# Optimization experiments

Hardware: AMD Instinct MI355X
Metric: run time of the kernel (lower is better)

Reference implementation:

```python
import jax, jax.numpy as jnp
import numpy as np

B, L, H2 = 64, 512, 1024  # batch, question length, 2*hidden_dim


def setup_inputs() -> dict:
    key = jax.random.key(0)
    ks = jax.random.split(key, 9)
    sc = 1.0 / np.sqrt(H2)
    return {
        "s_t_hat": jax.random.normal(ks[0], (B, H2), dtype=jnp.float32),
        "pai_q": jax.random.normal(ks[1], (B, L, H2), dtype=jnp.float32),
        "que_padding_mask": (jax.random.uniform(ks[2], (B, L)) > 0.1).astype(jnp.float32),
        "que_coverage": jax.random.uniform(ks[3], (B, L), dtype=jnp.float32),
        "W_q": jax.random.normal(ks[4], (H2, H2), dtype=jnp.float32) * sc,
        "W_qs_w": jax.random.normal(ks[5], (H2, H2), dtype=jnp.float32) * sc,
        "W_qs_b": jax.random.normal(ks[6], (H2,), dtype=jnp.float32) * sc,
        "W_c": jax.random.normal(ks[7], (1, H2), dtype=jnp.float32) * sc,
        "v_q": jax.random.normal(ks[8], (H2, 1), dtype=jnp.float32) * sc,
    }


def reference(s_t_hat, pai_q, que_padding_mask, que_coverage, W_q, W_qs_w, W_qs_b, W_c, v_q):
    # encoder feature: (b, l, 2h)
    enc_feat = jnp.einsum("blh,hk->blk", pai_q, W_q)
    # decoder feature: (b, 2h) -> broadcast over l
    dec_feat = s_t_hat @ W_qs_w + W_qs_b
    att = enc_feat + dec_feat[:, None, :]
    # coverage feature: (b, l, 1) @ (1, 2h)
    att = att + que_coverage[:, :, None] * W_c[0][None, None, :]
    e = jnp.tanh(att)                                  # (b, l, 2h)
    scores = jnp.einsum("blh,ho->bl", e, v_q)          # (b, l)
    alpha = jax.nn.softmax(scores, axis=1) * que_padding_mask
    alpha = alpha / jnp.sum(alpha, axis=1, keepdims=True)
    c_q_t = jnp.einsum("bl,blh->bh", alpha, pai_q)      # (b, 2h)
    new_cov = que_coverage + alpha
    return (c_q_t, alpha, new_cov)
```

## Files before the change

### kernel.cpp

```cpp
#include <hip/hip_runtime.h>
#include <hip/hip_bf16.h>

#define B_   64
#define L_   512
#define H2_  1024
#define M_   (B_ * L_)
#define KSPLIT 16
#define KCH  (H2_ / KSPLIT)

typedef short bf16x8 __attribute__((ext_vector_type(8)));
typedef float f32x4  __attribute__((ext_vector_type(4)));
typedef ushort ushort8_t __attribute__((ext_vector_type(8)));

__device__ __forceinline__ ushort f2bf(float f) {
    uint x = __float_as_uint(f);
    uint r = (x + 0x7FFFu + ((x >> 16) & 1u)) >> 16;
    return (ushort)r;
}

__device__ __forceinline__ float fast_tanh(float x) {
    float ax = fabsf(x);
    float e  = __expf(-2.0f * ax);
    float t  = 1.0f - 2.0f * e / (1.0f + e);
    return copysignf(t, x);
}

__device__ __forceinline__ void gload_lds16(const ushort* g, ushort* l) {
    __builtin_amdgcn_global_load_lds(
        (const __attribute__((address_space(1))) void*)g,
        (__attribute__((address_space(3))) void*)l, 16, 0, 0);
}

__global__ __launch_bounds__(256) void convertA_kernel(
    const float* __restrict__ in, ushort* __restrict__ out)
{
    size_t i = ((size_t)blockIdx.x * 256 + threadIdx.x) * 8;
    float4 a = *(const float4*)&in[i];
    float4 b = *(const float4*)&in[i + 4];
    ushort8_t h;
    h[0] = f2bf(a.x); h[1] = f2bf(a.y); h[2] = f2bf(a.z); h[3] = f2bf(a.w);
    h[4] = f2bf(b.x); h[5] = f2bf(b.y); h[6] = f2bf(b.z); h[7] = f2bf(b.w);
    *(ushort8_t*)&out[i] = h;
}

__global__ __launch_bounds__(256) void convertB_kernel(
    const float* __restrict__ W, ushort* __restrict__ out)
{
    __shared__ float t[32][33];
    int tx = threadIdx.x & 31, ty = threadIdx.x >> 5;
    int k0 = blockIdx.x * 32, n0 = blockIdx.y * 32;
    #pragma unroll
    for (int r = 0; r < 4; ++r)
        t[ty + r * 8][tx] = W[(size_t)(k0 + ty + r * 8) * H2_ + n0 + tx];
    __syncthreads();
    #pragma unroll
    for (int r = 0; r < 4; ++r)
        out[(size_t)(n0 + ty + r * 8) * H2_ + k0 + tx] = f2bf(t[tx][ty + r * 8]);
}

__global__ __launch_bounds__(256) void dec_split_kernel(
    const float* __restrict__ s_t_hat, const float* __restrict__ Wqs,
    float* __restrict__ dec_part)
{
    const int t  = threadIdx.x;
    const int n  = blockIdx.x * 64 + (t & 63);
    const int k0 = blockIdx.y * KCH;
    const int bg = t >> 6;

    float acc[16];
    #pragma unroll
    for (int i = 0; i < 16; ++i) acc[i] = 0.f;

    for (int k8 = 0; k8 < KCH; k8 += 8) {
        float w[8];
        #pragma unroll
        for (int kk = 0; kk < 8; ++kk)
            w[kk] = Wqs[(size_t)(k0 + k8 + kk) * H2_ + n];
        #pragma unroll
        for (int i = 0; i < 16; ++i) {
            const float* srow = &s_t_hat[(bg * 16 + i) * H2_ + k0 + k8];
            #pragma unroll
            for (int kk = 0; kk < 8; ++kk)
                acc[i] += srow[kk] * w[kk];
        }
    }
    #pragma unroll
    for (int i = 0; i < 16; ++i)
        dec_part[(size_t)blockIdx.y * (B_ * H2_) + (bg * 16 + i) * H2_ + n] = acc[i];
}

__global__ __launch_bounds__(256) void dec_reduce_kernel(
    const float* __restrict__ dec_part, const float* __restrict__ bqs,
    float* __restrict__ dec)
{
    int i = blockIdx.x * 256 + threadIdx.x;
    float s = bqs[i & (H2_ - 1)];
    #pragma unroll
    for (int p = 0; p < KSPLIT; ++p) s += dec_part[(size_t)p * (B_ * H2_) + i];
    dec[i] = s;
}

__global__ __launch_bounds__(256) void dec_kernel(
    const float* __restrict__ s_t_hat, const float* __restrict__ Wqs,
    const float* __restrict__ bqs, float* __restrict__ dec)
{
    int n  = blockIdx.x * 256 + threadIdx.x;
    int b0 = blockIdx.y * 4;
    float a0 = 0.f, a1 = 0.f, a2 = 0.f, a3 = 0.f;
    for (int h = 0; h < H2_; ++h) {
        float w = Wqs[h * H2_ + n];
        a0 += s_t_hat[(b0 + 0) * H2_ + h] * w;
        a1 += s_t_hat[(b0 + 1) * H2_ + h] * w;
        a2 += s_t_hat[(b0 + 2) * H2_ + h] * w;
        a3 += s_t_hat[(b0 + 3) * H2_ + h] * w;
    }
    float bias = bqs[n];
    dec[(b0 + 0) * H2_ + n] = a0 + bias;
    dec[(b0 + 1) * H2_ + n] = a1 + bias;
    dec[(b0 + 2) * H2_ + n] = a2 + bias;
    dec[(b0 + 3) * H2_ + n] = a3 + bias;
}

#define BM 128
#define BN 128
#define BK 64

__global__ __launch_bounds__(256) void score_kernel3(
    const ushort* __restrict__ Abf,
    const ushort* __restrict__ Bbf,
    const float* __restrict__ dec,
    const float* __restrict__ cov,
    const float* __restrict__ Wc,
    const float* __restrict__ vq,
    float* __restrict__ scores_part)
{
    __shared__ ushort As[BM * BK];
    __shared__ ushort Bs[BN * BK];

    const int tid  = threadIdx.x;
    const int lane = tid & 63;
    const int wave = tid >> 6;
    const int wm = wave >> 1, wn = wave & 1;
    const int m0 = blockIdx.x * BM;
    const int n0 = blockIdx.y * BN;

    f32x4 acc[4][4] = {};

    const int srow = lane >> 3;
    const int scol = ((lane & 7) ^ srow) * 8;
    const size_t abase = (size_t)(m0 + wave * 32 + srow) * H2_ + scol;
    const size_t bbase = (size_t)(n0 + wave * 32 + srow) * H2_ + scol;
    ushort* lA = As + wave * 32 * BK;
    ushort* lB = Bs + wave * 32 * BK;

    const int fr = lane & 15;
    const int fg = lane >> 4;
    const int fx = fr & 7;

    for (int kt = 0; kt < H2_; kt += BK) {
        #pragma unroll
        for (int p = 0; p < 4; ++p) {
            gload_lds16(Abf + abase + p * 8 * H2_ + kt, lA + p * 8 * BK);
            gload_lds16(Bbf + bbase + p * 8 * H2_ + kt, lB + p * 8 * BK);
        }
        __syncthreads();

        bf16x8 af[4][2];
        #pragma unroll
        for (int i = 0; i < 4; ++i)
            #pragma unroll
            for (int ks = 0; ks < 2; ++ks)
                af[i][ks] = *(const bf16x8*)
                    &As[(wm * 64 + i * 16 + fr) * BK + (((fg + ks * 4) ^ fx) * 8)];

        #pragma unroll
        for (int j = 0; j < 4; ++j) {
            bf16x8 b0 = *(const bf16x8*)
                &Bs[(wn * 64 + j * 16 + fr) * BK + ((fg ^ fx) * 8)];
            bf16x8 b1 = *(const bf16x8*)
                &Bs[(wn * 64 + j * 16 + fr) * BK + (((fg + 4) ^ fx) * 8)];
            #pragma unroll
            for (int i = 0; i < 4; ++i) {
                acc[i][j] = __builtin_amdgcn_mfma_f32_16x16x32_bf16(af[i][0], b0, acc[i][j], 0, 0, 0);
                acc[i][j] = __builtin_amdgcn_mfma_f32_16x16x32_bf16(af[i][1], b1, acc[i][j], 0, 0, 0);
            }
        }
        __syncthreads();
    }

    const int b = m0 >> 9;
    float dec4[4], wc4[4], vq4[4];
    #pragma unroll
    for (int j = 0; j < 4; ++j) {
        int n = n0 + wn * 64 + j * 16 + fr;
        dec4[j] = dec[b * H2_ + n];
        wc4[j]  = Wc[n];
        vq4[j]  = vq[n];
    }
    #pragma unroll
    for (int i = 0; i < 4; ++i) {
        #pragma unroll
        for (int r = 0; r < 4; ++r) {
            int ml = wm * 64 + i * 16 + fg * 4 + r;
            int m  = m0 + ml;
            float cv = cov[b * L_ + (m & (L_ - 1))];
            float s = 0.f;
            #pragma unroll
            for (int j = 0; j < 4; ++j) {
                float att = acc[i][j][r] + dec4[j] + cv * wc4[j];
                s += fast_tanh(att) * vq4[j];
            }
            s += __shfl_xor(s, 1);
            s += __shfl_xor(s, 2);
            s += __shfl_xor(s, 4);
            s += __shfl_xor(s, 8);
            if (fr == 0)
                scores_part[(size_t)(blockIdx.y * 2 + wn) * M_ + m] = s;
        }
    }
}

#define LDK 40
__global__ __launch_bounds__(256) void score_kernel_fb(
    const float* __restrict__ A, const float* __restrict__ Bmat,
    const float* __restrict__ dec, const float* __restrict__ cov,
    const float* __restrict__ Wc, const float* __restrict__ vq,
    float* __restrict__ scores_part)
{
    __shared__ ushort As[BM * LDK];
    __shared__ ushort Bs[BN * LDK];
    const int tid  = threadIdx.x;
    const int lane = tid & 63;
    const int wave = tid >> 6;
    const int wm = wave >> 1, wn = wave & 1;
    const int m0 = blockIdx.x * BM;
    const int n0 = blockIdx.y * BN;
    f32x4 acc[4][4] = {};
    const int a_row = tid >> 3;
    const int a_kc  = (tid & 7) * 4;
    const int b_k  = tid >> 5;
    const int b_nc = (tid & 31) * 4;
    const int fr = lane & 15;
    const int fg = lane >> 4;
    for (int kt = 0; kt < H2_; kt += 32) {
        #pragma unroll
        for (int p = 0; p < 4; ++p) {
            int row = a_row + p * 32;
            float4 v = *(const float4*)&A[(size_t)(m0 + row) * H2_ + kt + a_kc];
            ushort4 h;
            h.x = f2bf(v.x); h.y = f2bf(v.y); h.z = f2bf(v.z); h.w = f2bf(v.w);
            *(ushort4*)&As[row * LDK + a_kc] = h;
        }
        #pragma unroll
        for (int p = 0; p < 4; ++p) {
            int k = b_k + p * 8;
            float4 v = *(const float4*)&Bmat[(size_t)(kt + k) * H2_ + n0 + b_nc];
            Bs[(b_nc + 0) * LDK + k] = f2bf(v.x);
            Bs[(b_nc + 1) * LDK + k] = f2bf(v.y);
            Bs[(b_nc + 2) * LDK + k] = f2bf(v.z);
            Bs[(b_nc + 3) * LDK + k] = f2bf(v.w);
        }
        __syncthreads();
        bf16x8 af[4], bfr[4];
        #pragma unroll
        for (int i = 0; i < 4; ++i)
            af[i] = *(const bf16x8*)&As[(wm * 64 + i * 16 + fr) * LDK + fg * 8];
        #pragma unroll
        for (int j = 0; j < 4; ++j)
            bfr[j] = *(const bf16x8*)&Bs[(wn * 64 + j * 16 + fr) * LDK + fg * 8];
        #pragma unroll
        for (int i = 0; i < 4; ++i)
            #pragma unroll
            for (int j = 0; j < 4; ++j)
                acc[i][j] = __builtin_amdgcn_mfma_f32_16x16x32_bf16(af[i], bfr[j], acc[i][j], 0, 0, 0);
        __syncthreads();
    }
    const int b = m0 >> 9;
    float dec4[4], wc4[4], vq4[4];
    #pragma unroll
    for (int j = 0; j < 4; ++j) {
        int n = n0 + wn * 64 + j * 16 + fr;
        dec4[j] = dec[b * H2_ + n];
        wc4[j]  = Wc[n];
        vq4[j]  = vq[n];
    }
    #pragma unroll
    for (int i = 0; i < 4; ++i) {
        #pragma unroll
        for (int r = 0; r < 4; ++r) {
            int ml = wm * 64 + i * 16 + fg * 4 + r;
            int m  = m0 + ml;
            float cv = cov[b * L_ + (m & (L_ - 1))];
            float s = 0.f;
            #pragma unroll
            for (int j = 0; j < 4; ++j) {
                float att = acc[i][j][r] + dec4[j] + cv * wc4[j];
                s += fast_tanh(att) * vq4[j];
            }
            s += __shfl_xor(s, 1);
            s += __shfl_xor(s, 2);
            s += __shfl_xor(s, 4);
            s += __shfl_xor(s, 8);
            if (fr == 0)
                scores_part[(size_t)(blockIdx.y * 2 + wn) * M_ + m] = s;
        }
    }
}

__global__ __launch_bounds__(512) void softmax_kernel(
    const float* __restrict__ scores_part,
    const float* __restrict__ mask,
    const float* __restrict__ cov,
    float* __restrict__ out_alpha,
    float* __restrict__ out_newcov)
{
    int b = blockIdx.x;
    int l = threadIdx.x;
    int m = b * L_ + l;
    float s = 0.f;
    #pragma unroll
    for (int p = 0; p < 16; ++p) s += scores_part[(size_t)p * M_ + m];
    __shared__ float red[8];
    float mx = s;
    #pragma unroll
    for (int o = 1; o < 64; o <<= 1) mx = fmaxf(mx, __shfl_xor(mx, o));
    int wid = l >> 6;
    if ((l & 63) == 0) red[wid] = mx;
    __syncthreads();
    mx = red[0];
    #pragma unroll
    for (int p = 1; p < 8; ++p) mx = fmaxf(mx, red[p]);
    __syncthreads();
    float e = expf(s - mx) * mask[m];
    float sm = e;
    #pragma unroll
    for (int o = 1; o < 64; o <<= 1) sm += __shfl_xor(sm, o);
    if ((l & 63) == 0) red[wid] = sm;
    __syncthreads();
    float tot = 0.f;
    #pragma unroll
    for (int p = 0; p < 8; ++p) tot += red[p];
    float alpha = e / tot;
    out_alpha[m]  = alpha;
    out_newcov[m] = cov[m] + alpha;
}

__global__ __launch_bounds__(256) void cqt_bf_kernel(
    const float* __restrict__ alpha, const ushort* __restrict__ Abf,
    float* __restrict__ out)
{
    int b = blockIdx.y;
    int k = blockIdx.x * 256 + threadIdx.x;
    __shared__ float al[L_];
    al[threadIdx.x]       = alpha[b * L_ + threadIdx.x];
    al[threadIdx.x + 256] = alpha[b * L_ + threadIdx.x + 256];
    __syncthreads();
    float acc = 0.f;
    const ushort* p = &Abf[(size_t)b * L_ * H2_ + k];
    #pragma unroll 8
    for (int l = 0; l < L_; ++l) {
        float v = __uint_as_float((uint)p[(size_t)l * H2_] << 16);
        acc += al[l] * v;
    }
    out[b * H2_ + k] = acc;
}

__global__ __launch_bounds__(256) void cqt_kernel(
    const float* __restrict__ alpha, const float* __restrict__ pai_q,
    float* __restrict__ out)
{
    int b = blockIdx.y;
    int k = blockIdx.x * 256 + threadIdx.x;
    __shared__ float al[L_];
    al[threadIdx.x]       = alpha[b * L_ + threadIdx.x];
    al[threadIdx.x + 256] = alpha[b * L_ + threadIdx.x + 256];
    __syncthreads();
    float acc = 0.f;
    const float* p = &pai_q[(size_t)b * L_ * H2_ + k];
    #pragma unroll 8
    for (int l = 0; l < L_; ++l) acc += al[l] * p[(size_t)l * H2_];
    out[b * H2_ + k] = acc;
}

extern "C" void kernel_launch(void* const* d_in, const int* in_sizes, int n_in,
                              void* d_out, int out_size, void* d_ws, size_t ws_size,
                              hipStream_t stream)
{
    const float* s_t_hat = (const float*)d_in[0];
    const float* pai_q   = (const float*)d_in[1];
    const float* mask    = (const float*)d_in[2];
    const float* cov     = (const float*)d_in[3];
    const float* W_q     = (const float*)d_in[4];
    const float* W_qs_w  = (const float*)d_in[5];
    const float* W_qs_b  = (const float*)d_in[6];
    const float* W_c     = (const float*)d_in[7];
    const float* v_q     = (const float*)d_in[8];

    float* out     = (float*)d_out;
    float* c_q_t   = out;
    float* alpha   = out + B_ * H2_;
    float* newcov  = alpha + B_ * L_;

    char* ws = (char*)d_ws;
    float*  dec         = (float*)ws;
    float*  scores_part = (float*)(ws + 262144);
    ushort* Bbf         = (ushort*)(ws + 262144 + 2097152);
    ushort* Abf         = (ushort*)(ws + 262144 + 2097152 + 2097152);
    float*  dec_part    = (float*)Abf;
    const size_t ws_needed = 262144ull + 2097152ull + 2097152ull + 67108864ull;

    if (ws_size >= ws_needed) {
        dec_split_kernel<<<dim3(16, KSPLIT), 256, 0, stream>>>(s_t_hat, W_qs_w, dec_part);
        dec_reduce_kernel<<<dim3(B_ * H2_ / 256), 256, 0, stream>>>(dec_part, W_qs_b, dec);
        convertA_kernel<<<dim3((M_ * H2_) / (256 * 8)), 256, 0, stream>>>(pai_q, Abf);
        convertB_kernel<<<dim3(32, 32), 256, 0, stream>>>(W_q, Bbf);
        score_kernel3<<<dim3(M_ / BM, H2_ / BN), 256, 0, stream>>>(
            Abf, Bbf, dec, cov, W_c, v_q, scores_part);
        softmax_kernel<<<dim3(B_), 512, 0, stream>>>(scores_part, mask, cov, alpha, newcov);
        cqt_bf_kernel<<<dim3(4, B_), 256, 0, stream>>>(alpha, Abf, c_q_t);
    } else {
        dec_kernel<<<dim3(4, 16), 256, 0, stream>>>(s_t_hat, W_qs_w, W_qs_b, dec);
        score_kernel_fb<<<dim3(M_ / BM, H2_ / BN), 256, 0, stream>>>(
            pai_q, W_q, dec, cov, W_c, v_q, scores_part);
        softmax_kernel<<<dim3(B_), 512, 0, stream>>>(scores_part, mask, cov, alpha, newcov);
        cqt_kernel<<<dim3(4, B_), 256, 0, stream>>>(alpha, pai_q, c_q_t);
    }
}
```

Before: 186.4 us.

## Double-buffer LDS in score GEMM and remap blocks per XCD for reuse

The score GEMM kernel now uses two LDS buffers so the async global-to-LDS load of the next K tile overlaps MFMA compute on the current one, replacing the two full syncthreads per iteration with a vmcnt wait plus barriers. The launch grid becomes 1D and block IDs are remapped so each XCD handles a contiguous range of M blocks, with all 8 N blocks of an M row placed on the same XCD to improve L2 reuse of the A tiles. This doubles LDS use per block, which may reduce occupancy, and relies on a hand-placed vmcnt count that matches the number of outstanding loads.

```diff
diff --git a/kernel.cpp b/kernel.cpp
--- a/kernel.cpp
+++ b/kernel.cpp
@@ -125,7 +125,7 @@
 #define BN 128
 #define BK 64
 
-__global__ __launch_bounds__(256) void score_kernel3(
+__global__ __launch_bounds__(256) void score_kernel4(
     const ushort* __restrict__ Abf,
     const ushort* __restrict__ Bbf,
     const float* __restrict__ dec,
@@ -134,15 +134,21 @@
     const float* __restrict__ vq,
     float* __restrict__ scores_part)
 {
-    __shared__ ushort As[BM * BK];
-    __shared__ ushort Bs[BN * BK];
+    __shared__ ushort As[2][BM * BK];
+    __shared__ ushort Bs[2][BM * BK];
 
     const int tid  = threadIdx.x;
     const int lane = tid & 63;
     const int wave = tid >> 6;
     const int wm = wave >> 1, wn = wave & 1;
-    const int m0 = blockIdx.x * BM;
-    const int n0 = blockIdx.y * BN;
+
+    const int orig = blockIdx.x;
+    const int xcd  = orig & 7;
+    const int slot = orig >> 3;
+    const int mb   = xcd * 32 + (slot >> 3);
+    const int nb   = slot & 7;
+    const int m0 = mb * BM;
+    const int n0 = nb * BN;
 
     f32x4 acc[4][4] = {};
 
@@ -150,43 +156,56 @@
     const int scol = ((lane & 7) ^ srow) * 8;
     const size_t abase = (size_t)(m0 + wave * 32 + srow) * H2_ + scol;
     const size_t bbase = (size_t)(n0 + wave * 32 + srow) * H2_ + scol;
-    ushort* lA = As + wave * 32 * BK;
-    ushort* lB = Bs + wave * 32 * BK;
 
     const int fr = lane & 15;
     const int fg = lane >> 4;
     const int fx = fr & 7;
 
-    for (int kt = 0; kt < H2_; kt += BK) {
+    auto STAGE = [&](int kt, int bufsel) {
+        ushort* lA = &As[bufsel][wave * 32 * BK];
+        ushort* lB = &Bs[bufsel][wave * 32 * BK];
         #pragma unroll
         for (int p = 0; p < 4; ++p) {
             gload_lds16(Abf + abase + p * 8 * H2_ + kt, lA + p * 8 * BK);
             gload_lds16(Bbf + bbase + p * 8 * H2_ + kt, lB + p * 8 * BK);
         }
-        __syncthreads();
-
+    };
+
+    auto COMPUTE = [&](int bufsel) {
+        const ushort* Ab = As[bufsel];
+        const ushort* Bb = Bs[bufsel];
         bf16x8 af[4][2];
         #pragma unroll
         for (int i = 0; i < 4; ++i)
             #pragma unroll
             for (int ks = 0; ks < 2; ++ks)
                 af[i][ks] = *(const bf16x8*)
-                    &As[(wm * 64 + i * 16 + fr) * BK + (((fg + ks * 4) ^ fx) * 8)];
-
+                    &Ab[(wm * 64 + i * 16 + fr) * BK + (((fg + ks * 4) ^ fx) * 8)];
         #pragma unroll
         for (int j = 0; j < 4; ++j) {
             bf16x8 b0 = *(const bf16x8*)
-                &Bs[(wn * 64 + j * 16 + fr) * BK + ((fg ^ fx) * 8)];
+                &Bb[(wn * 64 + j * 16 + fr) * BK + ((fg ^ fx) * 8)];
             bf16x8 b1 = *(const bf16x8*)
-                &Bs[(wn * 64 + j * 16 + fr) * BK + (((fg + 4) ^ fx) * 8)];
+                &Bb[(wn * 64 + j * 16 + fr) * BK + (((fg + 4) ^ fx) * 8)];
             #pragma unroll
             for (int i = 0; i < 4; ++i) {
                 acc[i][j] = __builtin_amdgcn_mfma_f32_16x16x32_bf16(af[i][0], b0, acc[i][j], 0, 0, 0);
                 acc[i][j] = __builtin_amdgcn_mfma_f32_16x16x32_bf16(af[i][1], b1, acc[i][j], 0, 0, 0);
             }
         }
-        __syncthreads();
-    }
+    };
+
+    STAGE(0, 0);
+    for (int t = 0; t < 15; ++t) {
+        STAGE((t + 1) * BK, (t + 1) & 1);
+        asm volatile("s_waitcnt vmcnt(8)" ::: "memory");
+        __builtin_amdgcn_s_barrier();
+        COMPUTE(t & 1);
+        __builtin_amdgcn_s_barrier();
+    }
+    asm volatile("s_waitcnt vmcnt(0)" ::: "memory");
+    __builtin_amdgcn_s_barrier();
+    COMPUTE(1);
 
     const int b = m0 >> 9;
     float dec4[4], wc4[4], vq4[4];
@@ -215,7 +234,7 @@
             s += __shfl_xor(s, 4);
             s += __shfl_xor(s, 8);
             if (fr == 0)
-                scores_part[(size_t)(blockIdx.y * 2 + wn) * M_ + m] = s;
+                scores_part[(size_t)(nb * 2 + wn) * M_ + m] = s;
         }
     }
 }
@@ -414,7 +433,7 @@
         dec_reduce_kernel<<<dim3(B_ * H2_ / 256), 256, 0, stream>>>(dec_part, W_qs_b, dec);
         convertA_kernel<<<dim3((M_ * H2_) / (256 * 8)), 256, 0, stream>>>(pai_q, Abf);
         convertB_kernel<<<dim3(32, 32), 256, 0, stream>>>(W_q, Bbf);
-        score_kernel3<<<dim3(M_ / BM, H2_ / BN), 256, 0, stream>>>(
+        score_kernel4<<<dim3((M_ / BM) * (H2_ / BN)), 256, 0, stream>>>(
             Abf, Bbf, dec, cov, W_c, v_q, scores_part);
         softmax_kernel<<<dim3(B_), 512, 0, stream>>>(scores_part, mask, cov, alpha, newcov);
         cqt_bf_kernel<<<dim3(4, B_), 256, 0, stream>>>(alpha, Abf, c_q_t);
```

New measurement: 191.5 us. 2.7% more time.

## Replace score GEMM with 256x256 double-buffered, XCD-aware pipelined kernel

Applied to the files above, without the earlier changes.

The fused score GEMM now uses 256x256 tiles with BK=32, 512 threads and double-buffered LDS. Global-to-LDS prefetch of the next A and B tiles is interleaved with the MFMA phases, using explicit vmcnt waits, barriers and s_setprio. The 1D grid is remapped so each XCD works on a contiguous set of M-blocks, aiming for better L2 reuse. The aim is to hide load latency and raise arithmetic intensity, at the cost of higher register pressure and more barriers per k-step. The partial-score layout still yields 16 partials, so the softmax kernel is unchanged.

```diff
diff --git a/kernel.cpp b/kernel.cpp
--- a/kernel.cpp
+++ b/kernel.cpp
@@ -121,11 +121,11 @@
     dec[(b0 + 3) * H2_ + n] = a3 + bias;
 }
 
-#define BM 128
-#define BN 128
-#define BK 64
-
-__global__ __launch_bounds__(256) void score_kernel3(
+#define BM5 256
+#define BN5 256
+#define BK5 32
+
+__global__ __launch_bounds__(512, 2) void score_kernel5(
     const ushort* __restrict__ Abf,
     const ushort* __restrict__ Bbf,
     const float* __restrict__ dec,
@@ -134,60 +134,184 @@
     const float* __restrict__ vq,
     float* __restrict__ scores_part)
 {
-    __shared__ ushort As[BM * BK];
-    __shared__ ushort Bs[BN * BK];
-
+    __shared__ ushort As[2][BM5 * BK5];
+    __shared__ ushort Bs[2][BN5 * BK5];
+
+    const int tid  = threadIdx.x;
+    const int lane = tid & 63;
+    const int wave = tid >> 6;
+    const int wm   = wave >> 2;
+    const int wn   = wave & 3;
+
+    const int bid  = blockIdx.x;
+    const int xcd  = bid & 7;
+    const int slot = bid >> 3;
+    const int mb   = xcd * 16 + (slot >> 2);
+    const int nb   = slot & 3;
+    const int m0   = mb * BM5;
+    const int n0   = nb * BN5;
+
+    f32x4 acc[8][4] = {};
+
+    const int s_row = tid >> 2;
+    const int s_col = ((tid & 3) ^ ((s_row >> 1) & 3)) * 8;
+
+    const int fr = lane & 15;
+    const int fg = lane >> 4;
+    const int cA = ((fg ^ ((fr >> 1) & 3)) * 8);
+
+    #define STAGE_A(tile_) do {                                            \
+        ushort* lds_ = &As[(tile_) & 1][0];                                \
+        const ushort* gp_ = Abf + (size_t)(m0 + s_row) * H2_ + (tile_) * BK5 + s_col; \
+        gload_lds16(gp_,                     lds_ + wave * 512);           \
+        gload_lds16(gp_ + (size_t)128 * H2_, lds_ + 4096 + wave * 512);    \
+    } while (0)
+    #define STAGE_B(tile_) do {                                            \
+        ushort* lds_ = &Bs[(tile_) & 1][0];                                \
+        const ushort* gp_ = Bbf + (size_t)(n0 + s_row) * H2_ + (tile_) * BK5 + s_col; \
+        gload_lds16(gp_,                     lds_ + wave * 512);           \
+        gload_lds16(gp_ + (size_t)128 * H2_, lds_ + 4096 + wave * 512);    \
+    } while (0)
+
+    STAGE_B(0);
+    STAGE_A(0);
+    STAGE_B(1);
+    asm volatile("s_waitcnt vmcnt(2)" ::: "memory");
+    __builtin_amdgcn_s_barrier();
+
+    for (int u = 0; u < 32; ++u) {
+        const int cur = u & 1;
+        const ushort* Ab = &As[cur][0];
+        const ushort* Bb = &Bs[cur][0];
+        bf16x8 bfr[4];
+
+        #pragma unroll
+        for (int p = 0; p < 4; ++p) {
+            bf16x8 af0, af1;
+            if (p == 0) {
+                #pragma unroll
+                for (int j = 0; j < 4; ++j)
+                    bfr[j] = *(const bf16x8*)&Bb[(wn * 64 + j * 16 + fr) * BK5 + cA];
+                af0 = *(const bf16x8*)&Ab[(wm * 128 + 0 * 16 + fr) * BK5 + cA];
+                af1 = *(const bf16x8*)&Ab[(wm * 128 + 1 * 16 + fr) * BK5 + cA];
+                if (u < 31) STAGE_A(u + 1);
+            } else {
+                af0 = *(const bf16x8*)&Ab[(wm * 128 + (2 * p) * 16 + fr) * BK5 + cA];
+                af1 = *(const bf16x8*)&Ab[(wm * 128 + (2 * p + 1) * 16 + fr) * BK5 + cA];
+                if (p == 1 && u < 30) STAGE_B(u + 2);
+            }
+            __builtin_amdgcn_s_barrier();
+            __builtin_amdgcn_sched_barrier(0);
+            __builtin_amdgcn_s_setprio(1);
+            #pragma unroll
+            for (int j = 0; j < 4; ++j) {
+                acc[2 * p][j]     = __builtin_amdgcn_mfma_f32_16x16x32_bf16(af0, bfr[j], acc[2 * p][j], 0, 0, 0);
+                acc[2 * p + 1][j] = __builtin_amdgcn_mfma_f32_16x16x32_bf16(af1, bfr[j], acc[2 * p + 1][j], 0, 0, 0);
+            }
+            __builtin_amdgcn_s_setprio(0);
+            if (p < 3) {
+                __builtin_amdgcn_s_barrier();
+                __builtin_amdgcn_sched_barrier(0);
+            }
+        }
+        if (u < 31) {
+            if (u < 30) { asm volatile("s_waitcnt vmcnt(2)" ::: "memory"); }
+            else        { asm volatile("s_waitcnt vmcnt(0)" ::: "memory"); }
+            __builtin_amdgcn_s_barrier();
+            __builtin_amdgcn_sched_barrier(0);
+        }
+    }
+
+    const int b = mb >> 1;
+    float dec4[4], wc4[4], vq4[4];
+    #pragma unroll
+    for (int j = 0; j < 4; ++j) {
+        int n = n0 + wn * 64 + j * 16 + fr;
+        dec4[j] = dec[b * H2_ + n];
+        wc4[j]  = Wc[n];
+        vq4[j]  = vq[n];
+    }
+    #pragma unroll
+    for (int i = 0; i < 8; ++i) {
+        #pragma unroll
+        for (int r = 0; r < 4; ++r) {
+            int m = m0 + wm * 128 + i * 16 + fg * 4 + r;
+            float cv = cov[b * L_ + (m & (L_ - 1))];
+            float s = 0.f;
+            #pragma unroll
+            for (int j = 0; j < 4; ++j) {
+                float att = acc[i][j][r] + dec4[j] + cv * wc4[j];
+                s += fast_tanh(att) * vq4[j];
+            }
+            s += __shfl_xor(s, 1);
+            s += __shfl_xor(s, 2);
+            s += __shfl_xor(s, 4);
+            s += __shfl_xor(s, 8);
+            if (fr == 0)
+                scores_part[(size_t)(nb * 4 + wn) * M_ + m] = s;
+        }
+    }
+    #undef STAGE_A
+    #undef STAGE_B
+}
+
+#define BM 128
+#define BN 128
+#define LDK 40
+__global__ __launch_bounds__(256) void score_kernel_fb(
+    const float* __restrict__ A, const float* __restrict__ Bmat,
+    const float* __restrict__ dec, const float* __restrict__ cov,
+    const float* __restrict__ Wc, const float* __restrict__ vq,
+    float* __restrict__ scores_part)
+{
+    __shared__ ushort As[BM * LDK];
+    __shared__ ushort Bs[BN * LDK];
     const int tid  = threadIdx.x;
     const int lane = tid & 63;
     const int wave = tid >> 6;
     const int wm = wave >> 1, wn = wave & 1;
     const int m0 = blockIdx.x * BM;
     const int n0 = blockIdx.y * BN;
-
     f32x4 acc[4][4] = {};
-
-    const int srow = lane >> 3;
-    const int scol = ((lane & 7) ^ srow) * 8;
-    const size_t abase = (size_t)(m0 + wave * 32 + srow) * H2_ + scol;
-    const size_t bbase = (size_t)(n0 + wave * 32 + srow) * H2_ + scol;
-    ushort* lA = As + wave * 32 * BK;
-    ushort* lB = Bs + wave * 32 * BK;
-
+    const int a_row = tid >> 3;
+    const int a_kc  = (tid & 7) * 4;
+    const int b_k  = tid >> 5;
+    const int b_nc = (tid & 31) * 4;
     const int fr = lane & 15;
     const int fg = lane >> 4;
-    const int fx = fr & 7;
-
-    for (int kt = 0; kt < H2_; kt += BK) {
+    for (int kt = 0; kt < H2_; kt += 32) {
         #pragma unroll
         for (int p = 0; p < 4; ++p) {
-            gload_lds16(Abf + abase + p * 8 * H2_ + kt, lA + p * 8 * BK);
-            gload_lds16(Bbf + bbase + p * 8 * H2_ + kt, lB + p * 8 * BK);
+            int row = a_row + p * 32;
+            float4 v = *(const float4*)&A[(size_t)(m0 + row) * H2_ + kt + a_kc];
+            ushort4 h;
+            h.x = f2bf(v.x); h.y = f2bf(v.y); h.z = f2bf(v.z); h.w = f2bf(v.w);
+            *(ushort4*)&As[row * LDK + a_kc] = h;
+        }
+        #pragma unroll
+        for (int p = 0; p < 4; ++p) {
+            int k = b_k + p * 8;
+            float4 v = *(const float4*)&Bmat[(size_t)(kt + k) * H2_ + n0 + b_nc];
+            Bs[(b_nc + 0) * LDK + k] = f2bf(v.x);
+            Bs[(b_nc + 1) * LDK + k] = f2bf(v.y);
+            Bs[(b_nc + 2) * LDK + k] = f2bf(v.z);
+            Bs[(b_nc + 3) * LDK + k] = f2bf(v.w);
         }
         __syncthreads();
-
-        bf16x8 af[4][2];
+        bf16x8 af[4], bfr[4];
+        #pragma unroll
+        for (int i = 0; i < 4; ++i)
+            af[i] = *(const bf16x8*)&As[(wm * 64 + i * 16 + fr) * LDK + fg * 8];
+        #pragma unroll
+        for (int j = 0; j < 4; ++j)
+            bfr[j] = *(const bf16x8*)&Bs[(wn * 64 + j * 16 + fr) * LDK + fg * 8];
         #pragma unroll
         for (int i = 0; i < 4; ++i)
             #pragma unroll
-            for (int ks = 0; ks < 2; ++ks)
-                af[i][ks] = *(const bf16x8*)
-                    &As[(wm * 64 + i * 16 + fr) * BK + (((fg + ks * 4) ^ fx) * 8)];
-
-        #pragma unroll
-        for (int j = 0; j < 4; ++j) {
-            bf16x8 b0 = *(const bf16x8*)
-                &Bs[(wn * 64 + j * 16 + fr) * BK + ((fg ^ fx) * 8)];
-            bf16x8 b1 = *(const bf16x8*)
-                &Bs[(wn * 64 + j * 16 + fr) * BK + (((fg + 4) ^ fx) * 8)];
-            #pragma unroll
-            for (int i = 0; i < 4; ++i) {
-                acc[i][j] = __builtin_amdgcn_mfma_f32_16x16x32_bf16(af[i][0], b0, acc[i][j], 0, 0, 0);
-                acc[i][j] = __builtin_amdgcn_mfma_f32_16x16x32_bf16(af[i][1], b1, acc[i][j], 0, 0, 0);
-            }
-        }
+            for (int j = 0; j < 4; ++j)
+                acc[i][j] = __builtin_amdgcn_mfma_f32_16x16x32_bf16(af[i], bfr[j], acc[i][j], 0, 0, 0);
         __syncthreads();
     }
-
     const int b = m0 >> 9;
     float dec4[4], wc4[4], vq4[4];
     #pragma unroll
@@ -220,93 +344,6 @@
     }
 }
 
-#define LDK 40
-__global__ __launch_bounds__(256) void score_kernel_fb(
-    const float* __restrict__ A, const float* __restrict__ Bmat,
-    const float* __restrict__ dec, const float* __restrict__ cov,
-    const float* __restrict__ Wc, const float* __restrict__ vq,
-    float* __restrict__ scores_part)
-{
-    __shared__ ushort As[BM * LDK];
-    __shared__ ushort Bs[BN * LDK];
-    const int tid  = threadIdx.x;
-    const int lane = tid & 63;
-    const int wave = tid >> 6;
-    const int wm = wave >> 1, wn = wave & 1;
-    const int m0 = blockIdx.x * BM;
-    const int n0 = blockIdx.y * BN;
-    f32x4 acc[4][4] = {};
-    const int a_row = tid >> 3;
-    const int a_kc  = (tid & 7) * 4;
-    const int b_k  = tid >> 5;
-    const int b_nc = (tid & 31) * 4;
-    const int fr = lane & 15;
-    const int fg = lane >> 4;
-    for (int kt = 0; kt < H2_; kt += 32) {
-        #pragma unroll
-        for (int p = 0; p < 4; ++p) {
-            int row = a_row + p * 32;
-            float4 v = *(const float4*)&A[(size_t)(m0 + row) * H2_ + kt + a_kc];
-            ushort4 h;
-            h.x = f2bf(v.x); h.y = f2bf(v.y); h.z = f2bf(v.z); h.w = f2bf(v.w);
-            *(ushort4*)&As[row * LDK + a_kc] = h;
-        }
-        #pragma unroll
-        for (int p = 0; p < 4; ++p) {
-            int k = b_k + p * 8;
-            float4 v = *(const float4*)&Bmat[(size_t)(kt + k) * H2_ + n0 + b_nc];
-            Bs[(b_nc + 0) * LDK + k] = f2bf(v.x);
-            Bs[(b_nc + 1) * LDK + k] = f2bf(v.y);
-            Bs[(b_nc + 2) * LDK + k] = f2bf(v.z);
-            Bs[(b_nc + 3) * LDK + k] = f2bf(v.w);
-        }
-        __syncthreads();
-        bf16x8 af[4], bfr[4];
-        #pragma unroll
-        for (int i = 0; i < 4; ++i)
-            af[i] = *(const bf16x8*)&As[(wm * 64 + i * 16 + fr) * LDK + fg * 8];
-        #pragma unroll
-        for (int j = 0; j < 4; ++j)
-            bfr[j] = *(const bf16x8*)&Bs[(wn * 64 + j * 16 + fr) * LDK + fg * 8];
-        #pragma unroll
-        for (int i = 0; i < 4; ++i)
-            #pragma unroll
-            for (int j = 0; j < 4; ++j)
-                acc[i][j] = __builtin_amdgcn_mfma_f32_16x16x32_bf16(af[i], bfr[j], acc[i][j], 0, 0, 0);
-        __syncthreads();
-    }
-    const int b = m0 >> 9;
-    float dec4[4], wc4[4], vq4[4];
-    #pragma unroll
-    for (int j = 0; j < 4; ++j) {
-        int n = n0 + wn * 64 + j * 16 + fr;
-        dec4[j] = dec[b * H2_ + n];
-        wc4[j]  = Wc[n];
-        vq4[j]  = vq[n];
-    }
-    #pragma unroll
-    for (int i = 0; i < 4; ++i) {
-        #pragma unroll
-        for (int r = 0; r < 4; ++r) {
-            int ml = wm * 64 + i * 16 + fg * 4 + r;
-            int m  = m0 + ml;
-            float cv = cov[b * L_ + (m & (L_ - 1))];
-            float s = 0.f;
-            #pragma unroll
-            for (int j = 0; j < 4; ++j) {
-                float att = acc[i][j][r] + dec4[j] + cv * wc4[j];
-                s += fast_tanh(att) * vq4[j];
-            }
-            s += __shfl_xor(s, 1);
-            s += __shfl_xor(s, 2);
-            s += __shfl_xor(s, 4);
-            s += __shfl_xor(s, 8);
-            if (fr == 0)
-                scores_part[(size_t)(blockIdx.y * 2 + wn) * M_ + m] = s;
-        }
-    }
-}
-
 __global__ __launch_bounds__(512) void softmax_kernel(
     const float* __restrict__ scores_part,
     const float* __restrict__ mask,
@@ -414,7 +451,7 @@
         dec_reduce_kernel<<<dim3(B_ * H2_ / 256), 256, 0, stream>>>(dec_part, W_qs_b, dec);
         convertA_kernel<<<dim3((M_ * H2_) / (256 * 8)), 256, 0, stream>>>(pai_q, Abf);
         convertB_kernel<<<dim3(32, 32), 256, 0, stream>>>(W_q, Bbf);
-        score_kernel3<<<dim3(M_ / BM, H2_ / BN), 256, 0, stream>>>(
+        score_kernel5<<<dim3((M_ / BM5) * (H2_ / BN5)), 512, 0, stream>>>(
             Abf, Bbf, dec, cov, W_c, v_q, scores_part);
         softmax_kernel<<<dim3(B_), 512, 0, stream>>>(scores_part, mask, cov, alpha, newcov);
         cqt_bf_kernel<<<dim3(4, B_), 256, 0, stream>>>(alpha, Abf, c_q_t);
```

Result: slower. 200.4 us (+7.5%).

## Fuse fp32-to-bf16 conversion of pai_q into score GEMM with XCD-aware block mapping

Applied to the files above, without the earlier changes.

Removes the separate kernel that converted the whole 128MB fp32 activation into a 64MB bf16 copy. The GEMM now loads fp32 rows directly, converts them in registers and writes swizzled bf16 into LDS. A 1D grid is remapped so that blocks sharing the same M rows land on the same XCD, which should improve L2 reuse of the A tile. The context kernel now reads fp32 pai_q instead of the bf16 copy, and the workspace requirement shrinks. The cost is that A loads go through registers rather than direct-to-LDS loads, and each A tile is reloaded and reconverted by all 8 N-blocks.

```diff
diff --git a/kernel.cpp b/kernel.cpp
--- a/kernel.cpp
+++ b/kernel.cpp
@@ -29,18 +29,6 @@
     __builtin_amdgcn_global_load_lds(
         (const __attribute__((address_space(1))) void*)g,
         (__attribute__((address_space(3))) void*)l, 16, 0, 0);
-}
-
-__global__ __launch_bounds__(256) void convertA_kernel(
-    const float* __restrict__ in, ushort* __restrict__ out)
-{
-    size_t i = ((size_t)blockIdx.x * 256 + threadIdx.x) * 8;
-    float4 a = *(const float4*)&in[i];
-    float4 b = *(const float4*)&in[i + 4];
-    ushort8_t h;
-    h[0] = f2bf(a.x); h[1] = f2bf(a.y); h[2] = f2bf(a.z); h[3] = f2bf(a.w);
-    h[4] = f2bf(b.x); h[5] = f2bf(b.y); h[6] = f2bf(b.z); h[7] = f2bf(b.w);
-    *(ushort8_t*)&out[i] = h;
 }
 
 __global__ __launch_bounds__(256) void convertB_kernel(
@@ -121,12 +109,12 @@
     dec[(b0 + 3) * H2_ + n] = a3 + bias;
 }
 
-#define BM 128
-#define BN 128
-#define BK 64
-
-__global__ __launch_bounds__(256) void score_kernel3(
-    const ushort* __restrict__ Abf,
+#define BM6 128
+#define BN6 128
+#define BK6 64
+
+__global__ __launch_bounds__(256) void score_kernel6(
+    const float*  __restrict__ Afp,
     const ushort* __restrict__ Bbf,
     const float* __restrict__ dec,
     const float* __restrict__ cov,
@@ -134,34 +122,51 @@
     const float* __restrict__ vq,
     float* __restrict__ scores_part)
 {
-    __shared__ ushort As[BM * BK];
-    __shared__ ushort Bs[BN * BK];
+    __shared__ ushort As6[BM6 * BK6];
+    __shared__ ushort Bs6[BN6 * BK6];
 
     const int tid  = threadIdx.x;
     const int lane = tid & 63;
     const int wave = tid >> 6;
     const int wm = wave >> 1, wn = wave & 1;
-    const int m0 = blockIdx.x * BM;
-    const int n0 = blockIdx.y * BN;
+
+    const int bid  = blockIdx.x;
+    const int xcd  = bid & 7;
+    const int slot = bid >> 3;
+    const int mb   = xcd * 32 + (slot >> 3);
+    const int nbk  = slot & 7;
+    const int m0   = mb * BM6;
+    const int n0   = nbk * BN6;
 
     f32x4 acc[4][4] = {};
 
     const int srow = lane >> 3;
     const int scol = ((lane & 7) ^ srow) * 8;
-    const size_t abase = (size_t)(m0 + wave * 32 + srow) * H2_ + scol;
     const size_t bbase = (size_t)(n0 + wave * 32 + srow) * H2_ + scol;
-    ushort* lA = As + wave * 32 * BK;
-    ushort* lB = Bs + wave * 32 * BK;
+    ushort* lB = Bs6 + wave * 32 * BK6;
+
+    const int ar  = tid >> 3;
+    const int alc = tid & 7;
 
     const int fr = lane & 15;
     const int fg = lane >> 4;
     const int fx = fr & 7;
 
-    for (int kt = 0; kt < H2_; kt += BK) {
+    for (int kt = 0; kt < H2_; kt += BK6) {
+        #pragma unroll
+        for (int p = 0; p < 4; ++p)
+            gload_lds16(Bbf + bbase + (size_t)p * 8 * H2_ + kt, lB + p * 8 * BK6);
+
         #pragma unroll
         for (int p = 0; p < 4; ++p) {
-            gload_lds16(Abf + abase + p * 8 * H2_ + kt, lA + p * 8 * BK);
-            gload_lds16(Bbf + bbase + p * 8 * H2_ + kt, lB + p * 8 * BK);
+            int row = ar + p * 32;
+            const float* gp = &Afp[(size_t)(m0 + row) * H2_ + kt + alc * 8];
+            float4 v0 = *(const float4*)gp;
+            float4 v1 = *(const float4*)(gp + 4);
+            ushort8_t h;
+            h[0] = f2bf(v0.x); h[1] = f2bf(v0.y); h[2] = f2bf(v0.z); h[3] = f2bf(v0.w);
+            h[4] = f2bf(v1.x); h[5] = f2bf(v1.y); h[6] = f2bf(v1.z); h[7] = f2bf(v1.w);
+            *(ushort8_t*)&As6[row * BK6 + ((alc ^ (row & 7)) * 8)] = h;
         }
         __syncthreads();
 
@@ -171,14 +176,14 @@
             #pragma unroll
             for (int ks = 0; ks < 2; ++ks)
                 af[i][ks] = *(const bf16x8*)
-                    &As[(wm * 64 + i * 16 + fr) * BK + (((fg + ks * 4) ^ fx) * 8)];
+                    &As6[(wm * 64 + i * 16 + fr) * BK6 + (((fg + ks * 4) ^ fx) * 8)];
 
         #pragma unroll
         for (int j = 0; j < 4; ++j) {
             bf16x8 b0 = *(const bf16x8*)
-                &Bs[(wn * 64 + j * 16 + fr) * BK + ((fg ^ fx) * 8)];
+                &Bs6[(wn * 64 + j * 16 + fr) * BK6 + ((fg ^ fx) * 8)];
             bf16x8 b1 = *(const bf16x8*)
-                &Bs[(wn * 64 + j * 16 + fr) * BK + (((fg + 4) ^ fx) * 8)];
+                &Bs6[(wn * 64 + j * 16 + fr) * BK6 + (((fg + 4) ^ fx) * 8)];
             #pragma unroll
             for (int i = 0; i < 4; ++i) {
                 acc[i][j] = __builtin_amdgcn_mfma_f32_16x16x32_bf16(af[i][0], b0, acc[i][j], 0, 0, 0);
@@ -215,11 +220,13 @@
             s += __shfl_xor(s, 4);
             s += __shfl_xor(s, 8);
             if (fr == 0)
-                scores_part[(size_t)(blockIdx.y * 2 + wn) * M_ + m] = s;
-        }
-    }
-}
-
+                scores_part[(size_t)(nbk * 2 + wn) * M_ + m] = s;
+        }
+    }
+}
+
+#define BM 128
+#define BN 128
 #define LDK 40
 __global__ __launch_bounds__(256) void score_kernel_fb(
     const float* __restrict__ A, const float* __restrict__ Bmat,
@@ -345,26 +352,6 @@
     out_newcov[m] = cov[m] + alpha;
 }
 
-__global__ __launch_bounds__(256) void cqt_bf_kernel(
-    const float* __restrict__ alpha, const ushort* __restrict__ Abf,
-    float* __restrict__ out)
-{
-    int b = blockIdx.y;
-    int k = blockIdx.x * 256 + threadIdx.x;
-    __shared__ float al[L_];
-    al[threadIdx.x]       = alpha[b * L_ + threadIdx.x];
-    al[threadIdx.x + 256] = alpha[b * L_ + threadIdx.x + 256];
-    __syncthreads();
-    float acc = 0.f;
-    const ushort* p = &Abf[(size_t)b * L_ * H2_ + k];
-    #pragma unroll 8
-    for (int l = 0; l < L_; ++l) {
-        float v = __uint_as_float((uint)p[(size_t)l * H2_] << 16);
-        acc += al[l] * v;
-    }
-    out[b * H2_ + k] = acc;
-}
-
 __global__ __launch_bounds__(256) void cqt_kernel(
     const float* __restrict__ alpha, const float* __restrict__ pai_q,
     float* __restrict__ out)
@@ -405,20 +392,19 @@
     float*  dec         = (float*)ws;
     float*  scores_part = (float*)(ws + 262144);
     ushort* Bbf         = (ushort*)(ws + 262144 + 2097152);
-    ushort* Abf         = (ushort*)(ws + 262144 + 2097152 + 2097152);
-    float*  dec_part    = (float*)Abf;
-    const size_t ws_needed = 262144ull + 2097152ull + 2097152ull + 67108864ull;
+    float*  dec_part    = (float*)(ws + 262144 + 2097152 + 2097152);
+    const size_t ws_needed = 262144ull + 2097152ull + 2097152ull + 4194304ull;
+    const size_t ws_min_fb = 262144ull + 2097152ull;
 
     if (ws_size >= ws_needed) {
         dec_split_kernel<<<dim3(16, KSPLIT), 256, 0, stream>>>(s_t_hat, W_qs_w, dec_part);
         dec_reduce_kernel<<<dim3(B_ * H2_ / 256), 256, 0, stream>>>(dec_part, W_qs_b, dec);
-        convertA_kernel<<<dim3((M_ * H2_) / (256 * 8)), 256, 0, stream>>>(pai_q, Abf);
         convertB_kernel<<<dim3(32, 32), 256, 0, stream>>>(W_q, Bbf);
-        score_kernel3<<<dim3(M_ / BM, H2_ / BN), 256, 0, stream>>>(
-            Abf, Bbf, dec, cov, W_c, v_q, scores_part);
+        score_kernel6<<<dim3((M_ / BM6) * (H2_ / BN6)), 256, 0, stream>>>(
+            pai_q, Bbf, dec, cov, W_c, v_q, scores_part);
         softmax_kernel<<<dim3(B_), 512, 0, stream>>>(scores_part, mask, cov, alpha, newcov);
-        cqt_bf_kernel<<<dim3(4, B_), 256, 0, stream>>>(alpha, Abf, c_q_t);
-    } else {
+        cqt_kernel<<<dim3(4, B_), 256, 0, stream>>>(alpha, pai_q, c_q_t);
+    } else if (ws_size >= ws_min_fb) {
         dec_kernel<<<dim3(4, 16), 256, 0, stream>>>(s_t_hat, W_qs_w, W_qs_b, dec);
         score_kernel_fb<<<dim3(M_ / BM, H2_ / BN), 256, 0, stream>>>(
             pai_q, W_q, dec, cov, W_c, v_q, scores_part);
```

Result: slower. 191.2 us (+2.6%).
